# Performance work log

Measured on AMD Instinct MI355X. Metric: run time of the kernel, lower is better.

The kernel has to match this reference:

```python
import jax, jax.numpy as jnp
import numpy as np

NNODES = 512   # sensors/nodes
WIN    = 64    # window_size (input features per node)
NH     = 64    # nhidden
NG     = 3     # ngnn iterations
BATCH  = 1024
OUT    = 32    # out_channels
EPS    = 1e-5  # BatchNorm1d eps


def setup_inputs() -> dict:
    key = jax.random.key(0)
    ks = jax.random.split(key, 8)
    X = jax.random.normal(ks[0], (BATCH, NNODES, WIN), jnp.float32)
    adj_const = jax.random.uniform(ks[1], (NNODES, NNODES), jnp.float32)
    # GCN layer 1 per gnn-iteration: window -> nhidden
    W1 = 0.05 * jax.random.normal(ks[2], (NG, WIN, NH), jnp.float32)
    b1 = jnp.zeros((NG, NH), jnp.float32)
    g1 = jnp.ones((NG, NNODES), jnp.float32)
    be1 = jnp.zeros((NG, NNODES), jnp.float32)
    # GCN layer 2 per gnn-iteration: nhidden -> nhidden
    W2 = 0.05 * jax.random.normal(ks[3], (NG, NH, NH), jnp.float32)
    b2 = jnp.zeros((NG, NH), jnp.float32)
    g2 = jnp.ones((NG, NNODES), jnp.float32)
    be2 = jnp.zeros((NG, NNODES), jnp.float32)
    Wfc = 0.05 * jax.random.normal(ks[4], (NG * NH, OUT), jnp.float32)
    bfc = jnp.zeros((OUT,), jnp.float32)
    return dict(X=X, adj_const=adj_const, W1=W1, b1=b1, g1=g1, be1=be1,
                W2=W2, b2=b2, g2=g2, be2=be2, Wfc=Wfc, bfc=bfc)


def _bn_nodes(h, gamma, beta):
    # torch BatchNorm1d(nnodes) on [B, N, F]: normalize per node channel over (B, F)
    mean = jnp.mean(h, axis=(0, 2), keepdims=True)
    var = jnp.var(h, axis=(0, 2), keepdims=True)
    return (h - mean) * jax.lax.rsqrt(var + EPS) * gamma[None, :, None] + beta[None, :, None]


def reference(X, adj_const, W1, b1, g1, be1, W2, b2, g2, be2, Wfc, bfc):
    # ConstantGraph returns the constant adjacency; z = ones - eye kills self-loops
    adj = adj_const * (1.0 - jnp.eye(NNODES, dtype=X.dtype))
    outs = []
    for i in range(NG):
        # GCNLayer: aggregate over neighbors then linear project
        h = jnp.einsum('nm,bmw->bnw', adj, X) @ W1[i] + b1[i]   # [B,N,NH]
        h = jax.nn.relu(h)
        h = _bn_nodes(h, g1[i], be1[i])
        skip = jnp.min(h, axis=1)                                # [B,NH]
        h = jnp.einsum('nm,bmd->bnd', adj, h) @ W2[i] + b2[i]
        h = jax.nn.relu(h)
        h = _bn_nodes(h, g2[i], be2[i])
        outs.append(jnp.min(h, axis=1) + skip)                   # [B,NH]
    h = jnp.concatenate(outs, axis=1)                            # [B, NG*NH]
    return h @ Wfc + bfc
```

## Files before the change

### kernel.cpp

```cpp
#include <hip/hip_runtime.h>


typedef short  s16x8 __attribute__((ext_vector_type(8)));
typedef float  f32x4 __attribute__((ext_vector_type(4)));

#define NN   512
#define NB   1024
#define NH   64
#define LDT  72

#define MFMA16(a, b, c) __builtin_amdgcn_mfma_f32_16x16x32_bf16((a), (b), (c), 0, 0, 0)

#define GLOAD16(g, l) __builtin_amdgcn_global_load_lds( \
    (const __attribute__((address_space(1))) unsigned*)(g), \
    (__attribute__((address_space(3))) unsigned*)(l), 16, 0, 0)

__device__ __forceinline__ unsigned short f2bf(float f) {
  union { float f; unsigned u; } v; v.f = f;
  unsigned r = v.u + 0x7fffu + ((v.u >> 16) & 1u);
  return (unsigned short)(r >> 16);
}
__device__ __forceinline__ float bf2f(unsigned short h) {
  union { unsigned u; float f; } v; v.u = ((unsigned)h) << 16;
  return v.f;
}

__global__ void k_prep_adj(const float* __restrict__ adj, unsigned short* __restrict__ adjbf) {
  int idx = blockIdx.x * 256 + threadIdx.x;
  int n = idx >> 9, m = idx & 511;
  float v = adj[idx];
  if (n == m) v = 0.f;
  adjbf[idx] = f2bf(v);
}

__global__ void k_prep_w(const float* __restrict__ W1, const float* __restrict__ W2,
                         unsigned short* __restrict__ W1t, unsigned short* __restrict__ W2t) {
  int idx = blockIdx.x * 256 + threadIdx.x;
  int i = idx >> 12, rc_ = idx & 4095;
  int src = (i << 12) + ((rc_ & 63) << 6) + (rc_ >> 6);
  W1t[idx] = f2bf(W1[src]);
  W2t[idx] = f2bf(W2[src]);
}

__global__ __launch_bounds__(256)
void k_transpose_x(const float* __restrict__ X, unsigned short* __restrict__ Xt) {
  __shared__ unsigned short T[64 * LDT];
  int blk = blockIdx.x; int b = blk >> 3; int m0 = (blk & 7) << 6;
  int t = threadIdx.x; int r = t >> 2, seg = t & 3;
  const float* src = X + ((size_t)b * NN + m0 + r) * NH + seg * 16;
#pragma unroll
  for (int e = 0; e < 16; ++e) T[(seg * 16 + e) * LDT + r] = f2bf(src[e]);
  __syncthreads();
  unsigned short* dst = Xt + ((size_t)b * NH + r) * NN + m0 + seg * 16;
  const unsigned short* sT = &T[r * LDT + seg * 16];
  *(s16x8*)dst       = *(const s16x8*)sT;
  *(s16x8*)(dst + 8) = *(const s16x8*)(sT + 8);
}

__global__ __launch_bounds__(512)
void k_gnn1(const unsigned short* __restrict__ Xt, const unsigned short* __restrict__ adjbf,
            const unsigned short* __restrict__ W1t, const float* __restrict__ b1,
            unsigned short* __restrict__ H1T, float* __restrict__ SS1, float* __restrict__ SQ1) {
  __shared__ unsigned short Ab[2][2][4096];
  __shared__ unsigned short Bb[2][8192];
  int h = blockIdx.x;
  int blk = (h & 7) * 256 + (h >> 3);
  int bp = blk >> 2, n0 = (blk & 3) << 7;
  int b0 = bp * 2, b1v = bp * 2 + 1;
  int t = threadIdx.x, lane = t & 63, wid = t >> 6;
  int wf = wid & 1, wn = wid >> 1;
  int arow = wid * 8 + (lane >> 3);
  int swz = ((lane & 7) ^ (arow & 7)) << 3;
  const unsigned short* aS0 = Xt + ((size_t)b0  * NH + arow) * NN + swz;
  const unsigned short* aS1 = Xt + ((size_t)b1v * NH + arow) * NN + swz;
  const unsigned short* bS0 = adjbf + (size_t)(n0 + arow) * NN + swz;
  const unsigned short* bS1 = adjbf + (size_t)(n0 + 64 + arow) * NN + swz;

  GLOAD16(aS0, &Ab[0][0][wid * 512]);
  GLOAD16(aS1, &Ab[1][0][wid * 512]);
  GLOAD16(bS0, &Bb[0][wid * 512]);
  GLOAD16(bS1, &Bb[0][4096 + wid * 512]);
  __syncthreads();

  f32x4 acc[2][2][2] = {};
  for (int kt = 0; kt < 8; ++kt) {
    int cur = kt & 1;
    if (kt < 7) {
      int off = (kt + 1) * 64;
      GLOAD16(aS0 + off, &Ab[0][cur ^ 1][wid * 512]);
      GLOAD16(aS1 + off, &Ab[1][cur ^ 1][wid * 512]);
      GLOAD16(bS0 + off, &Bb[cur ^ 1][wid * 512]);
      GLOAD16(bS1 + off, &Bb[cur ^ 1][4096 + wid * 512]);
    }
    const unsigned short* B = Bb[cur];
#pragma unroll
    for (int kk = 0; kk < 2; ++kk) {
      int ks = (lane >> 4) + kk * 4;
      int ra0 = wf * 32 + (lane & 15), ra1 = ra0 + 16;
      int rb0 = wn * 32 + (lane & 15), rb1 = rb0 + 16;
      s16x8 bf0 = *(const s16x8*)&B[rb0 * 64 + ((ks ^ (rb0 & 7)) << 3)];
      s16x8 bf1 = *(const s16x8*)&B[rb1 * 64 + ((ks ^ (rb1 & 7)) << 3)];
#pragma unroll
      for (int bs = 0; bs < 2; ++bs) {
        const unsigned short* A = Ab[bs][cur];
        s16x8 a0 = *(const s16x8*)&A[ra0 * 64 + ((ks ^ (ra0 & 7)) << 3)];
        s16x8 a1 = *(const s16x8*)&A[ra1 * 64 + ((ks ^ (ra1 & 7)) << 3)];
        acc[bs][0][0] = MFMA16(a0, bf0, acc[bs][0][0]);
        acc[bs][1][0] = MFMA16(a1, bf0, acc[bs][1][0]);
        acc[bs][0][1] = MFMA16(a0, bf1, acc[bs][0][1]);
        acc[bs][1][1] = MFMA16(a1, bf1, acc[bs][1][1]);
      }
    }
    __syncthreads();
  }
#pragma unroll
  for (int bs = 0; bs < 2; ++bs) {
    unsigned short* T = Bb[bs];
#pragma unroll
    for (int fi = 0; fi < 2; ++fi)
#pragma unroll
      for (int fj = 0; fj < 2; ++fj) {
        int nl = wn * 32 + fj * 16 + (lane & 15);
        int w0 = wf * 32 + fi * 16 + (lane >> 4) * 4;
        ushort4 p;
        p.x = f2bf(acc[bs][fi][fj][0]); p.y = f2bf(acc[bs][fi][fj][1]);
        p.z = f2bf(acc[bs][fi][fj][2]); p.w = f2bf(acc[bs][fi][fj][3]);
        *(ushort4*)&T[nl * 64 + (((w0 >> 3) ^ (nl & 7)) << 3) + (w0 & 7)] = p;
      }
  }
#pragma unroll
  for (int j = 0; j < 3; ++j) {
    unsigned short* dstp = (j == 0) ? &Ab[0][0][wid * 512]
                         : (j == 1) ? &Ab[0][1][wid * 512] : &Ab[1][0][wid * 512];
    const unsigned short* gsrc = W1t + j * 4096 + (wid * 8 + (lane >> 3)) * 64
                               + (((lane & 7) ^ (lane >> 3)) << 3);
    GLOAD16(gsrc, dstp);
  }
  __syncthreads();
  int nrow = wid * 16 + (lane & 15);
  s16x8 aT[2][2];
#pragma unroll
  for (int bs = 0; bs < 2; ++bs)
#pragma unroll
    for (int kk = 0; kk < 2; ++kk) {
      int ks = (lane >> 4) + kk * 4;
      aT[bs][kk] = *(const s16x8*)&Bb[bs][nrow * 64 + ((ks ^ (nrow & 7)) << 3)];
    }
#pragma unroll
  for (int i = 0; i < 3; ++i) {
    const unsigned short* w1p = (i == 0) ? Ab[0][0] : (i == 1) ? Ab[0][1] : Ab[1][0];
    s16x8 bw[2][4];
#pragma unroll
    for (int kk = 0; kk < 2; ++kk) {
      int ks = (lane >> 4) + kk * 4;
#pragma unroll
      for (int fd = 0; fd < 4; ++fd) {
        int fr = fd * 16 + (lane & 15);
        bw[kk][fd] = *(const s16x8*)&w1p[fr * 64 + ((ks ^ (fr & 7)) << 3)];
      }
    }
    f32x4 acc2[2][4] = {};
#pragma unroll
    for (int bs = 0; bs < 2; ++bs)
#pragma unroll
      for (int kk = 0; kk < 2; ++kk) {
        acc2[bs][0] = MFMA16(aT[bs][kk], bw[kk][0], acc2[bs][0]);
        acc2[bs][1] = MFMA16(aT[bs][kk], bw[kk][1], acc2[bs][1]);
        acc2[bs][2] = MFMA16(aT[bs][kk], bw[kk][2], acc2[bs][2]);
        acc2[bs][3] = MFMA16(aT[bs][kk], bw[kk][3], acc2[bs][3]);
      }
    unsigned short* H1i = H1T + (size_t)i * 33554432u;
    float svr[4] = {0.f, 0.f, 0.f, 0.f}, sqr[4] = {0.f, 0.f, 0.f, 0.f};
#pragma unroll
    for (int bs = 0; bs < 2; ++bs) {
      int bcur = bs == 0 ? b0 : b1v;
#pragma unroll
      for (int fd = 0; fd < 4; ++fd) {
        int f = fd * 16 + (lane & 15);
        float bia = b1[i * 64 + f];
        float x0 = fmaxf(acc2[bs][fd][0] + bia, 0.f);
        float x1 = fmaxf(acc2[bs][fd][1] + bia, 0.f);
        float x2 = fmaxf(acc2[bs][fd][2] + bia, 0.f);
        float x3 = fmaxf(acc2[bs][fd][3] + bia, 0.f);
        svr[0] += x0; svr[1] += x1; svr[2] += x2; svr[3] += x3;
        sqr[0] += x0 * x0; sqr[1] += x1 * x1; sqr[2] += x2 * x2; sqr[3] += x3 * x3;
        ushort4 p;
        p.x = f2bf(x0); p.y = f2bf(x1); p.z = f2bf(x2); p.w = f2bf(x3);
        *(ushort4*)&H1i[((size_t)bcur * NH + f) * NN + n0 + nrow - (lane & 15) + (lane >> 4) * 4] = p;
      }
    }
#pragma unroll
    for (int rr = 0; rr < 4; ++rr) {
      float sv = svr[rr], qv = sqr[rr];
      sv += __shfl_xor(sv, 1); sv += __shfl_xor(sv, 2); sv += __shfl_xor(sv, 4); sv += __shfl_xor(sv, 8);
      qv += __shfl_xor(qv, 1); qv += __shfl_xor(qv, 2); qv += __shfl_xor(qv, 4); qv += __shfl_xor(qv, 8);
      if ((lane & 15) == 0) {
        int n = n0 + wid * 16 + (lane >> 4) * 4 + rr;
        atomicAdd(&SS1[i * 512 + n], sv);
        atomicAdd(&SQ1[i * 512 + n], qv);
      }
    }
  }
}

__global__ __launch_bounds__(256)
void k_adjb(const unsigned short* __restrict__ adjbf,
            const float* __restrict__ Ssum, const float* __restrict__ Ssq,
            const float* __restrict__ g, const float* __restrict__ be,
            unsigned short* __restrict__ adjB, float* __restrict__ rc,
            float* __restrict__ A1, float* __restrict__ C1) {
  __shared__ float red[256];
  int n = blockIdx.x, t = threadIdx.x;
  float acc = 0.f;
#pragma unroll
  for (int hh = 0; hh < 2; ++hh) {
    int m = t + hh * 256;
    float mean = Ssum[m] * (1.f / 65536.f);
    float var  = Ssq[m] * (1.f / 65536.f) - mean * mean;
    float a = g[m] * rsqrtf(var + 1e-5f);
    float c = be[m] - mean * a;
    if (n == 0) { A1[m] = a; C1[m] = c; }
    float av = bf2f(adjbf[n * NN + m]);
    adjB[n * NN + m] = f2bf(av * a);
    acc += av * c;
  }
  red[t] = acc; __syncthreads();
  for (int s = 128; s > 0; s >>= 1) { if (t < s) red[t] += red[t + s]; __syncthreads(); }
  if (t == 0) rc[n] = red[0];
}

__global__ __launch_bounds__(256)
void k_minrow_out(const unsigned short* __restrict__ Ht,
                  const float* __restrict__ Ssum, const float* __restrict__ Ssq,
                  const float* __restrict__ g, const float* __restrict__ be,
                  const float* __restrict__ skip_i, float* __restrict__ outs, int i) {
  int t = threadIdx.x, lane = t & 63, wid = t >> 6;
  int row = blockIdx.x * 4 + wid;
  int b = row >> 6, d = row & 63;
  s16x8 hv = *(const s16x8*)(Ht + (size_t)row * NN + lane * 8);
  float m = 1e30f;
#pragma unroll
  for (int e = 0; e < 8; ++e) {
    int mm = lane * 8 + e;
    float mean = Ssum[mm] * (1.f / 65536.f);
    float var  = Ssq[mm] * (1.f / 65536.f) - mean * mean;
    float a = g[mm] * rsqrtf(var + 1e-5f);
    float c = be[mm] - mean * a;
    m = fminf(m, a * bf2f((unsigned short)hv[e]) + c);
  }
#pragma unroll
  for (int off = 1; off < 64; off <<= 1) m = fminf(m, __shfl_xor(m, off));
  if (lane == 0) outs[(size_t)b * 192 + i * 64 + d] = m + skip_i[row];
}

__global__ __launch_bounds__(512)
void k_layer2(const unsigned short* __restrict__ H1t_i, const unsigned short* __restrict__ adjB,
              const float* __restrict__ rc, const unsigned short* __restrict__ W2t_i,
              const float* __restrict__ b2_i, unsigned short* __restrict__ H2t,
              float* __restrict__ Ssum2, float* __restrict__ Ssq2,
              const float* __restrict__ A1v, const float* __restrict__ C1v,
              float* __restrict__ skip_i) {
  __shared__ unsigned short Ab[2][2][4096];
  __shared__ unsigned short Bb[2][8192];
  __shared__ float acs[512], ccs[512];
  int h = blockIdx.x;
  int blk = (h & 7) * 256 + (h >> 3);
  int bp = blk >> 2, n0 = (blk & 3) << 7;
  int b0 = bp * 2, b1v = bp * 2 + 1;
  int t = threadIdx.x, lane = t & 63, wid = t >> 6;
  int wf = wid & 1, wn = wid >> 1;
  bool do_min = (n0 == 0);
  int arow = wid * 8 + (lane >> 3);
  int swz = ((lane & 7) ^ (arow & 7)) << 3;
  const unsigned short* aS0 = H1t_i + ((size_t)b0  * NH + arow) * NN + swz;
  const unsigned short* aS1 = H1t_i + ((size_t)b1v * NH + arow) * NN + swz;
  const unsigned short* bS0 = adjB + (size_t)(n0 + arow) * NN + swz;
  const unsigned short* bS1 = adjB + (size_t)(n0 + 64 + arow) * NN + swz;
  acs[t] = A1v[t]; ccs[t] = C1v[t];
  float rcv[2];
  rcv[0] = rc[n0 + wn * 32 + (lane & 15)];
  rcv[1] = rc[n0 + wn * 32 + 16 + (lane & 15)];

  GLOAD16(aS0, &Ab[0][0][wid * 512]);
  GLOAD16(aS1, &Ab[1][0][wid * 512]);
  GLOAD16(bS0, &Bb[0][wid * 512]);
  GLOAD16(bS1, &Bb[0][4096 + wid * 512]);
  __syncthreads();

  float mn0 = 1e30f, mn1 = 1e30f;
  f32x4 acc[2][2][2] = {};
  for (int kt = 0; kt < 8; ++kt) {
    int cur = kt & 1;
    if (kt < 7) {
      int off = (kt + 1) * 64;
      GLOAD16(aS0 + off, &Ab[0][cur ^ 1][wid * 512]);
      GLOAD16(aS1 + off, &Ab[1][cur ^ 1][wid * 512]);
      GLOAD16(bS0 + off, &Bb[cur ^ 1][wid * 512]);
      GLOAD16(bS1 + off, &Bb[cur ^ 1][4096 + wid * 512]);
    }
    if (do_min) {
      int s2 = ((lane & 7) ^ (arow & 7)) << 3;
      s16x8 av0 = *(const s16x8*)&Ab[0][cur][arow * 64 + s2];
      s16x8 av1 = *(const s16x8*)&Ab[1][cur][arow * 64 + s2];
      int m0 = kt * 64 + ((lane & 7) << 3);
#pragma unroll
      for (int e = 0; e < 8; ++e) {
        mn0 = fminf(mn0, acs[m0 + e] * bf2f((unsigned short)av0[e]) + ccs[m0 + e]);
        mn1 = fminf(mn1, acs[m0 + e] * bf2f((unsigned short)av1[e]) + ccs[m0 + e]);
      }
    }
    const unsigned short* B = Bb[cur];
#pragma unroll
    for (int kk = 0; kk < 2; ++kk) {
      int ks = (lane >> 4) + kk * 4;
      int ra0 = wf * 32 + (lane & 15), ra1 = ra0 + 16;
      int rb0 = wn * 32 + (lane & 15), rb1 = rb0 + 16;
      s16x8 bf0 = *(const s16x8*)&B[rb0 * 64 + ((ks ^ (rb0 & 7)) << 3)];
      s16x8 bf1 = *(const s16x8*)&B[rb1 * 64 + ((ks ^ (rb1 & 7)) << 3)];
#pragma unroll
      for (int bs = 0; bs < 2; ++bs) {
        const unsigned short* A = Ab[bs][cur];
        s16x8 a0 = *(const s16x8*)&A[ra0 * 64 + ((ks ^ (ra0 & 7)) << 3)];
        s16x8 a1 = *(const s16x8*)&A[ra1 * 64 + ((ks ^ (ra1 & 7)) << 3)];
        acc[bs][0][0] = MFMA16(a0, bf0, acc[bs][0][0]);
        acc[bs][1][0] = MFMA16(a1, bf0, acc[bs][1][0]);
        acc[bs][0][1] = MFMA16(a0, bf1, acc[bs][0][1]);
        acc[bs][1][1] = MFMA16(a1, bf1, acc[bs][1][1]);
      }
    }
    __syncthreads();
  }
  if (do_min) {
    mn0 = fminf(mn0, __shfl_xor(mn0, 1)); mn1 = fminf(mn1, __shfl_xor(mn1, 1));
    mn0 = fminf(mn0, __shfl_xor(mn0, 2)); mn1 = fminf(mn1, __shfl_xor(mn1, 2));
    mn0 = fminf(mn0, __shfl_xor(mn0, 4)); mn1 = fminf(mn1, __shfl_xor(mn1, 4));
    if ((lane & 7) == 0) {
      skip_i[b0 * 64 + arow] = mn0;
      skip_i[b1v * 64 + arow] = mn1;
    }
  }
#pragma unroll
  for (int bs = 0; bs < 2; ++bs) {
    unsigned short* Gt = Bb[bs];
#pragma unroll
    for (int fi = 0; fi < 2; ++fi)
#pragma unroll
      for (int fj = 0; fj < 2; ++fj) {
        int n  = wn * 32 + fj * 16 + (lane & 15);
        int f0 = wf * 32 + fi * 16 + (lane >> 4) * 4;
        ushort4 p;
        p.x = f2bf(acc[bs][fi][fj][0] + rcv[fj]); p.y = f2bf(acc[bs][fi][fj][1] + rcv[fj]);
        p.z = f2bf(acc[bs][fi][fj][2] + rcv[fj]); p.w = f2bf(acc[bs][fi][fj][3] + rcv[fj]);
        *(ushort4*)&Gt[n * 64 + (((f0 >> 3) ^ (n & 7)) << 3) + (f0 & 7)] = p;
      }
  }
  __syncthreads();
  s16x8 w2f[2][4];
  float bb[4];
#pragma unroll
  for (int kk = 0; kk < 2; ++kk)
#pragma unroll
    for (int fd = 0; fd < 4; ++fd)
      w2f[kk][fd] = *(const s16x8*)&W2t_i[(fd * 16 + (lane & 15)) * 64 + kk * 32 + (lane >> 4) * 8];
#pragma unroll
  for (int fd = 0; fd < 4; ++fd) bb[fd] = b2_i[fd * 16 + (lane & 15)];

  int nrow = wid * 16 + (lane & 15);
  f32x4 acc2[2][4] = {};
#pragma unroll
  for (int bs = 0; bs < 2; ++bs)
#pragma unroll
    for (int kk = 0; kk < 2; ++kk) {
      int ks = (lane >> 4) + kk * 4;
      s16x8 a = *(const s16x8*)&Bb[bs][nrow * 64 + ((ks ^ (nrow & 7)) << 3)];
      acc2[bs][0] = MFMA16(a, w2f[kk][0], acc2[bs][0]);
      acc2[bs][1] = MFMA16(a, w2f[kk][1], acc2[bs][1]);
      acc2[bs][2] = MFMA16(a, w2f[kk][2], acc2[bs][2]);
      acc2[bs][3] = MFMA16(a, w2f[kk][3], acc2[bs][3]);
    }
  float svr[4] = {0.f, 0.f, 0.f, 0.f}, sqr[4] = {0.f, 0.f, 0.f, 0.f};
#pragma unroll
  for (int bs = 0; bs < 2; ++bs) {
    int bcur = bs == 0 ? b0 : b1v;
#pragma unroll
    for (int fd = 0; fd < 4; ++fd) {
      int d  = fd * 16 + (lane & 15);
      int nw = n0 + wid * 16 + (lane >> 4) * 4;
      float x0 = fmaxf(acc2[bs][fd][0] + bb[fd], 0.f);
      float x1 = fmaxf(acc2[bs][fd][1] + bb[fd], 0.f);
      float x2 = fmaxf(acc2[bs][fd][2] + bb[fd], 0.f);
      float x3 = fmaxf(acc2[bs][fd][3] + bb[fd], 0.f);
      svr[0] += x0; svr[1] += x1; svr[2] += x2; svr[3] += x3;
      sqr[0] += x0 * x0; sqr[1] += x1 * x1; sqr[2] += x2 * x2; sqr[3] += x3 * x3;
      ushort4 p;
      p.x = f2bf(x0); p.y = f2bf(x1); p.z = f2bf(x2); p.w = f2bf(x3);
      *(ushort4*)&H2t[((size_t)bcur * NH + d) * NN + nw] = p;
    }
  }
#pragma unroll
  for (int rr = 0; rr < 4; ++rr) {
    float sv = svr[rr], qv = sqr[rr];
    sv += __shfl_xor(sv, 1); sv += __shfl_xor(sv, 2); sv += __shfl_xor(sv, 4); sv += __shfl_xor(sv, 8);
    qv += __shfl_xor(qv, 1); qv += __shfl_xor(qv, 2); qv += __shfl_xor(qv, 4); qv += __shfl_xor(qv, 8);
    if ((lane & 15) == 0) {
      int n = n0 + wid * 16 + (lane >> 4) * 4 + rr;
      atomicAdd(&Ssum2[n], sv);
      atomicAdd(&Ssq2[n], qv);
    }
  }
}

__global__ __launch_bounds__(256)
void k_fc(const float* __restrict__ outs, const float* __restrict__ Wfc,
          const float* __restrict__ bfc, float* __restrict__ out) {
  int t = threadIdx.x;
  int b = blockIdx.x * 8 + (t >> 5), o = t & 31;
  float acc = bfc[o];
  const float* orow = outs + (size_t)b * 192;
  for (int j = 0; j < 192; ++j) acc += orow[j] * Wfc[j * 32 + o];
  out[b * 32 + o] = acc;
}

extern "C" void kernel_launch(void* const* d_in, const int* in_sizes, int n_in,
                              void* d_out, int out_size, void* d_ws, size_t ws_size,
                              hipStream_t stream) {
  const float* X   = (const float*)d_in[0];
  const float* adj = (const float*)d_in[1];
  const float* W1  = (const float*)d_in[2];
  const float* b1  = (const float*)d_in[3];
  const float* g1  = (const float*)d_in[4];
  const float* be1 = (const float*)d_in[5];
  const float* W2  = (const float*)d_in[6];
  const float* b2  = (const float*)d_in[7];
  const float* g2  = (const float*)d_in[8];
  const float* be2 = (const float*)d_in[9];
  const float* Wfc = (const float*)d_in[10];
  const float* bfc = (const float*)d_in[11];
  float* out = (float*)d_out;

  char* ws = (char*)d_ws;
  size_t off = 0;
  auto alloc = [&](size_t bytes) {
    char* p = ws + off; off += (bytes + 255) & ~(size_t)255; return p;
  };
  unsigned short* ADJBF = (unsigned short*)alloc(512 * 512 * 2);
  unsigned short* ADJB  = (unsigned short*)alloc(512 * 512 * 2);
  unsigned short* W1T   = (unsigned short*)alloc(3 * 4096 * 2);
  unsigned short* W2T   = (unsigned short*)alloc(3 * 4096 * 2);
  float* SS1 = (float*)alloc(3 * 512 * 4);
  float* SQ1 = (float*)alloc(3 * 512 * 4);
  float* SS2 = (float*)alloc(3 * 512 * 4);
  float* SQ2 = (float*)alloc(3 * 512 * 4);
  float* A1  = (float*)alloc(3 * 512 * 4);
  float* C1  = (float*)alloc(3 * 512 * 4);
  float* RC  = (float*)alloc(512 * 4);
  float* SKIP = (float*)alloc(3 * 1024 * 64 * 4);
  float* OUTS = (float*)alloc(1024 * 192 * 4);
  unsigned short* XT  = (unsigned short*)alloc((size_t)1024 * 64 * 512 * 2);
  unsigned short* H1T = (unsigned short*)alloc((size_t)3 * 1024 * 64 * 512 * 2);
  unsigned short* H2T = XT;

  hipMemsetAsync(SS1, 0, 4 * 3 * 512 * 4, stream);

  k_prep_adj<<<1024, 256, 0, stream>>>(adj, ADJBF);
  k_prep_w<<<48, 256, 0, stream>>>(W1, W2, W1T, W2T);
  k_transpose_x<<<8192, 256, 0, stream>>>(X, XT);
  k_gnn1<<<2048, 512, 0, stream>>>(XT, ADJBF, W1T, b1, H1T, SS1, SQ1);

  for (int i = 0; i < 3; ++i) {
    k_adjb<<<512, 256, 0, stream>>>(ADJBF, SS1 + i * 512, SQ1 + i * 512,
                                    g1 + i * 512, be1 + i * 512, ADJB, RC,
                                    A1 + i * 512, C1 + i * 512);
    k_layer2<<<2048, 512, 0, stream>>>(H1T + (size_t)i * 33554432u, ADJB, RC,
                                       W2T + i * 4096, b2 + i * 64, H2T,
                                       SS2 + i * 512, SQ2 + i * 512,
                                       A1 + i * 512, C1 + i * 512, SKIP + i * 65536);
    k_minrow_out<<<16384, 256, 0, stream>>>(H2T, SS2 + i * 512, SQ2 + i * 512,
                                            g2 + i * 512, be2 + i * 512,
                                            SKIP + i * 65536, OUTS, i);
  }
  k_fc<<<128, 256, 0, stream>>>(OUTS, Wfc, bfc, out);
}
```

Measured before the change: 531.2 us.

## Recompute layer-1 hidden in layer2 from shared aggregate instead of storing H1

```diff
diff --git a/kernel.cpp b/kernel.cpp
--- a/kernel.cpp
+++ b/kernel.cpp
@@ -60,7 +60,7 @@
 __global__ __launch_bounds__(512)
 void k_gnn1(const unsigned short* __restrict__ Xt, const unsigned short* __restrict__ adjbf,
             const unsigned short* __restrict__ W1t, const float* __restrict__ b1,
-            unsigned short* __restrict__ H1T, float* __restrict__ SS1, float* __restrict__ SQ1) {
+            unsigned short* __restrict__ Tg, float* __restrict__ SS1, float* __restrict__ SQ1) {
   __shared__ unsigned short Ab[2][2][4096];
   __shared__ unsigned short Bb[2][8192];
   int h = blockIdx.x;
@@ -115,6 +115,21 @@
   }
 #pragma unroll
   for (int bs = 0; bs < 2; ++bs) {
+    int bcur = bs == 0 ? b0 : b1v;
+#pragma unroll
+    for (int fi = 0; fi < 2; ++fi)
+#pragma unroll
+      for (int fj = 0; fj < 2; ++fj) {
+        int n = n0 + wn * 32 + fj * 16 + (lane & 15);
+        int w = wf * 32 + fi * 16 + (lane >> 4) * 4;
+        ushort4 pk;
+        pk.x = f2bf(acc[bs][fi][fj][0]); pk.y = f2bf(acc[bs][fi][fj][1]);
+        pk.z = f2bf(acc[bs][fi][fj][2]); pk.w = f2bf(acc[bs][fi][fj][3]);
+        *(ushort4*)&Tg[((size_t)bcur * NN + n) * NH + w] = pk;
+      }
+  }
+#pragma unroll
+  for (int bs = 0; bs < 2; ++bs) {
     unsigned short* T = Bb[bs];
 #pragma unroll
     for (int fi = 0; fi < 2; ++fi)
@@ -169,26 +184,18 @@
         acc2[bs][2] = MFMA16(aT[bs][kk], bw[kk][2], acc2[bs][2]);
         acc2[bs][3] = MFMA16(aT[bs][kk], bw[kk][3], acc2[bs][3]);
       }
-    unsigned short* H1i = H1T + (size_t)i * 33554432u;
     float svr[4] = {0.f, 0.f, 0.f, 0.f}, sqr[4] = {0.f, 0.f, 0.f, 0.f};
 #pragma unroll
-    for (int bs = 0; bs < 2; ++bs) {
-      int bcur = bs == 0 ? b0 : b1v;
+    for (int bs = 0; bs < 2; ++bs)
 #pragma unroll
       for (int fd = 0; fd < 4; ++fd) {
-        int f = fd * 16 + (lane & 15);
-        float bia = b1[i * 64 + f];
-        float x0 = fmaxf(acc2[bs][fd][0] + bia, 0.f);
-        float x1 = fmaxf(acc2[bs][fd][1] + bia, 0.f);
-        float x2 = fmaxf(acc2[bs][fd][2] + bia, 0.f);
-        float x3 = fmaxf(acc2[bs][fd][3] + bia, 0.f);
-        svr[0] += x0; svr[1] += x1; svr[2] += x2; svr[3] += x3;
-        sqr[0] += x0 * x0; sqr[1] += x1 * x1; sqr[2] += x2 * x2; sqr[3] += x3 * x3;
-        ushort4 p;
-        p.x = f2bf(x0); p.y = f2bf(x1); p.z = f2bf(x2); p.w = f2bf(x3);
-        *(ushort4*)&H1i[((size_t)bcur * NH + f) * NN + n0 + nrow - (lane & 15) + (lane >> 4) * 4] = p;
-      }
-    }
+        float bia = b1[i * 64 + fd * 16 + (lane & 15)];
+#pragma unroll
+        for (int rr = 0; rr < 4; ++rr) {
+          float x = fmaxf(acc2[bs][fd][rr] + bia, 0.f);
+          svr[rr] += x; sqr[rr] += x * x;
+        }
+      }
 #pragma unroll
     for (int rr = 0; rr < 4; ++rr) {
       float sv = svr[rr], qv = sqr[rr];
@@ -253,107 +260,136 @@
   if (lane == 0) outs[(size_t)b * 192 + i * 64 + d] = m + skip_i[row];
 }
 
-__global__ __launch_bounds__(512)
-void k_layer2(const unsigned short* __restrict__ H1t_i, const unsigned short* __restrict__ adjB,
-              const float* __restrict__ rc, const unsigned short* __restrict__ W2t_i,
-              const float* __restrict__ b2_i, unsigned short* __restrict__ H2t,
+__global__ __launch_bounds__(256)
+void k_layer2(const unsigned short* __restrict__ Tg, const unsigned short* __restrict__ adjB,
+              const float* __restrict__ rc,
+              const unsigned short* __restrict__ W1t_i, const float* __restrict__ b1_i,
+              const unsigned short* __restrict__ W2t_i, const float* __restrict__ b2_i,
+              unsigned short* __restrict__ H2t,
               float* __restrict__ Ssum2, float* __restrict__ Ssq2,
               const float* __restrict__ A1v, const float* __restrict__ C1v,
               float* __restrict__ skip_i) {
-  __shared__ unsigned short Ab[2][2][4096];
+  __shared__ unsigned short Tch[2][4096];
   __shared__ unsigned short Bb[2][8192];
+  __shared__ unsigned short H1c[4096];
   __shared__ float acs[512], ccs[512];
   int h = blockIdx.x;
-  int blk = (h & 7) * 256 + (h >> 3);
-  int bp = blk >> 2, n0 = (blk & 3) << 7;
-  int b0 = bp * 2, b1v = bp * 2 + 1;
+  int blk = (h & 7) * 512 + (h >> 3);
+  int b = blk >> 2, n0 = (blk & 3) << 7;
   int t = threadIdx.x, lane = t & 63, wid = t >> 6;
   int wf = wid & 1, wn = wid >> 1;
   bool do_min = (n0 == 0);
-  int arow = wid * 8 + (lane >> 3);
-  int swz = ((lane & 7) ^ (arow & 7)) << 3;
-  const unsigned short* aS0 = H1t_i + ((size_t)b0  * NH + arow) * NN + swz;
-  const unsigned short* aS1 = H1t_i + ((size_t)b1v * NH + arow) * NN + swz;
-  const unsigned short* bS0 = adjB + (size_t)(n0 + arow) * NN + swz;
-  const unsigned short* bS1 = adjB + (size_t)(n0 + 64 + arow) * NN + swz;
-  acs[t] = A1v[t]; ccs[t] = C1v[t];
-  float rcv[2];
-  rcv[0] = rc[n0 + wn * 32 + (lane & 15)];
-  rcv[1] = rc[n0 + wn * 32 + 16 + (lane & 15)];
-
-  GLOAD16(aS0, &Ab[0][0][wid * 512]);
-  GLOAD16(aS1, &Ab[1][0][wid * 512]);
-  GLOAD16(bS0, &Bb[0][wid * 512]);
-  GLOAD16(bS1, &Bb[0][4096 + wid * 512]);
+  acs[t] = A1v[t]; acs[t + 256] = A1v[t + 256];
+  ccs[t] = C1v[t]; ccs[t + 256] = C1v[t + 256];
+  s16x8 w1f[2];
+  float b1r[4];
+#pragma unroll
+  for (int kk = 0; kk < 2; ++kk)
+    w1f[kk] = *(const s16x8*)&W1t_i[(wid * 16 + (lane & 15)) * 64 + kk * 32 + (lane >> 4) * 8];
+#pragma unroll
+  for (int rr = 0; rr < 4; ++rr) b1r[rr] = b1_i[wid * 16 + (lane >> 4) * 4 + rr];
+  int lrow = lane >> 3, lsl = lane & 7;
+  const unsigned short* tBase = Tg + (size_t)b * (NN * NH);
+#pragma unroll
+  for (int q = 0; q < 2; ++q) {
+    int r = wid * 16 + q * 8 + lrow;
+    GLOAD16(tBase + (size_t)r * NH + ((lsl ^ (r & 7)) << 3), &Tch[0][r * 64]);
+  }
+#pragma unroll
+  for (int q = 0; q < 4; ++q) {
+    int r = wid * 32 + q * 8 + lrow;
+    GLOAD16(adjB + (size_t)(n0 + r) * NN + ((lsl ^ (r & 7)) << 3), &Bb[0][r * 64]);
+  }
   __syncthreads();
 
-  float mn0 = 1e30f, mn1 = 1e30f;
-  f32x4 acc[2][2][2] = {};
+  float mn[4] = {1e30f, 1e30f, 1e30f, 1e30f};
+  f32x4 acc[2][4] = {};
   for (int kt = 0; kt < 8; ++kt) {
     int cur = kt & 1;
     if (kt < 7) {
-      int off = (kt + 1) * 64;
-      GLOAD16(aS0 + off, &Ab[0][cur ^ 1][wid * 512]);
-      GLOAD16(aS1 + off, &Ab[1][cur ^ 1][wid * 512]);
-      GLOAD16(bS0 + off, &Bb[cur ^ 1][wid * 512]);
-      GLOAD16(bS1 + off, &Bb[cur ^ 1][4096 + wid * 512]);
-    }
-    if (do_min) {
-      int s2 = ((lane & 7) ^ (arow & 7)) << 3;
-      s16x8 av0 = *(const s16x8*)&Ab[0][cur][arow * 64 + s2];
-      s16x8 av1 = *(const s16x8*)&Ab[1][cur][arow * 64 + s2];
-      int m0 = kt * 64 + ((lane & 7) << 3);
-#pragma unroll
-      for (int e = 0; e < 8; ++e) {
-        mn0 = fminf(mn0, acs[m0 + e] * bf2f((unsigned short)av0[e]) + ccs[m0 + e]);
-        mn1 = fminf(mn1, acs[m0 + e] * bf2f((unsigned short)av1[e]) + ccs[m0 + e]);
-      }
-    }
-    const unsigned short* B = Bb[cur];
-#pragma unroll
-    for (int kk = 0; kk < 2; ++kk) {
-      int ks = (lane >> 4) + kk * 4;
-      int ra0 = wf * 32 + (lane & 15), ra1 = ra0 + 16;
-      int rb0 = wn * 32 + (lane & 15), rb1 = rb0 + 16;
-      s16x8 bf0 = *(const s16x8*)&B[rb0 * 64 + ((ks ^ (rb0 & 7)) << 3)];
-      s16x8 bf1 = *(const s16x8*)&B[rb1 * 64 + ((ks ^ (rb1 & 7)) << 3)];
-#pragma unroll
-      for (int bs = 0; bs < 2; ++bs) {
-        const unsigned short* A = Ab[bs][cur];
-        s16x8 a0 = *(const s16x8*)&A[ra0 * 64 + ((ks ^ (ra0 & 7)) << 3)];
-        s16x8 a1 = *(const s16x8*)&A[ra1 * 64 + ((ks ^ (ra1 & 7)) << 3)];
-        acc[bs][0][0] = MFMA16(a0, bf0, acc[bs][0][0]);
-        acc[bs][1][0] = MFMA16(a1, bf0, acc[bs][1][0]);
-        acc[bs][0][1] = MFMA16(a0, bf1, acc[bs][0][1]);
-        acc[bs][1][1] = MFMA16(a1, bf1, acc[bs][1][1]);
+      int koff = (kt + 1) * 64;
+#pragma unroll
+      for (int q = 0; q < 2; ++q) {
+        int r = wid * 16 + q * 8 + lrow;
+        GLOAD16(tBase + (size_t)(koff + r) * NH + ((lsl ^ (r & 7)) << 3), &Tch[cur ^ 1][r * 64]);
+      }
+#pragma unroll
+      for (int q = 0; q < 4; ++q) {
+        int r = wid * 32 + q * 8 + lrow;
+        GLOAD16(adjB + (size_t)(n0 + r) * NN + koff + ((lsl ^ (r & 7)) << 3), &Bb[cur ^ 1][r * 64]);
+      }
+    }
+    {
+      const unsigned short* Tc = Tch[cur];
+#pragma unroll
+      for (int mt = 0; mt < 4; ++mt) {
+        f32x4 rg = {};
+#pragma unroll
+        for (int kk = 0; kk < 2; ++kk) {
+          int ks = (lane >> 4) + kk * 4;
+          int mr = mt * 16 + (lane & 15);
+          s16x8 tf = *(const s16x8*)&Tc[mr * 64 + ((ks ^ (mr & 7)) << 3)];
+          rg = MFMA16(w1f[kk], tf, rg);
+        }
+        int mloc = mt * 16 + (lane & 15);
+        int mglob = kt * 64 + mloc;
+        float ac = acs[mglob], cc = ccs[mglob];
+#pragma unroll
+        for (int rr = 0; rr < 4; ++rr) {
+          float x = fmaxf(rg[rr] + b1r[rr], 0.f);
+          if (do_min) mn[rr] = fminf(mn[rr], ac * x + cc);
+          int f = wid * 16 + (lane >> 4) * 4 + rr;
+          H1c[f * 64 + (((mloc >> 3) ^ (f & 7)) << 3) + (mloc & 7)] = f2bf(x);
+        }
       }
     }
     __syncthreads();
+    {
+      const unsigned short* B = Bb[cur];
+#pragma unroll
+      for (int kk = 0; kk < 2; ++kk) {
+        int ks = (lane >> 4) + kk * 4;
+        int ra0 = wf * 32 + (lane & 15), ra1 = ra0 + 16;
+        s16x8 a0 = *(const s16x8*)&H1c[ra0 * 64 + ((ks ^ (ra0 & 7)) << 3)];
+        s16x8 a1 = *(const s16x8*)&H1c[ra1 * 64 + ((ks ^ (ra1 & 7)) << 3)];
+#pragma unroll
+        for (int j = 0; j < 4; ++j) {
+          int rb = wn * 64 + j * 16 + (lane & 15);
+          s16x8 bf = *(const s16x8*)&B[rb * 64 + ((ks ^ (rb & 7)) << 3)];
+          acc[0][j] = MFMA16(a0, bf, acc[0][j]);
+          acc[1][j] = MFMA16(a1, bf, acc[1][j]);
+        }
+      }
+    }
+    __syncthreads();
   }
   if (do_min) {
-    mn0 = fminf(mn0, __shfl_xor(mn0, 1)); mn1 = fminf(mn1, __shfl_xor(mn1, 1));
-    mn0 = fminf(mn0, __shfl_xor(mn0, 2)); mn1 = fminf(mn1, __shfl_xor(mn1, 2));
-    mn0 = fminf(mn0, __shfl_xor(mn0, 4)); mn1 = fminf(mn1, __shfl_xor(mn1, 4));
-    if ((lane & 7) == 0) {
-      skip_i[b0 * 64 + arow] = mn0;
-      skip_i[b1v * 64 + arow] = mn1;
-    }
-  }
-#pragma unroll
-  for (int bs = 0; bs < 2; ++bs) {
-    unsigned short* Gt = Bb[bs];
-#pragma unroll
-    for (int fi = 0; fi < 2; ++fi)
-#pragma unroll
-      for (int fj = 0; fj < 2; ++fj) {
-        int n  = wn * 32 + fj * 16 + (lane & 15);
-        int f0 = wf * 32 + fi * 16 + (lane >> 4) * 4;
-        ushort4 p;
-        p.x = f2bf(acc[bs][fi][fj][0] + rcv[fj]); p.y = f2bf(acc[bs][fi][fj][1] + rcv[fj]);
-        p.z = f2bf(acc[bs][fi][fj][2] + rcv[fj]); p.w = f2bf(acc[bs][fi][fj][3] + rcv[fj]);
-        *(ushort4*)&Gt[n * 64 + (((f0 >> 3) ^ (n & 7)) << 3) + (f0 & 7)] = p;
-      }
-  }
+#pragma unroll
+    for (int rr = 0; rr < 4; ++rr) {
+      mn[rr] = fminf(mn[rr], __shfl_xor(mn[rr], 1));
+      mn[rr] = fminf(mn[rr], __shfl_xor(mn[rr], 2));
+      mn[rr] = fminf(mn[rr], __shfl_xor(mn[rr], 4));
+      mn[rr] = fminf(mn[rr], __shfl_xor(mn[rr], 8));
+    }
+    if ((lane & 15) == 0) {
+#pragma unroll
+      for (int rr = 0; rr < 4; ++rr)
+        skip_i[b * 64 + wid * 16 + (lane >> 4) * 4 + rr] = mn[rr];
+    }
+  }
+  unsigned short* Gt = Bb[0];
+#pragma unroll
+  for (int fi = 0; fi < 2; ++fi)
+#pragma unroll
+    for (int j = 0; j < 4; ++j) {
+      int n  = wn * 64 + j * 16 + (lane & 15);
+      int f0 = wf * 32 + fi * 16 + (lane >> 4) * 4;
+      float rv = rc[n0 + n];
+      ushort4 p;
+      p.x = f2bf(acc[fi][j][0] + rv); p.y = f2bf(acc[fi][j][1] + rv);
+      p.z = f2bf(acc[fi][j][2] + rv); p.w = f2bf(acc[fi][j][3] + rv);
+      *(ushort4*)&Gt[n * 64 + (((f0 >> 3) ^ (n & 7)) << 3) + (f0 & 7)] = p;
+    }
   __syncthreads();
   s16x8 w2f[2][4];
   float bb[4];
@@ -365,47 +401,43 @@
 #pragma unroll
   for (int fd = 0; fd < 4; ++fd) bb[fd] = b2_i[fd * 16 + (lane & 15)];
 
-  int nrow = wid * 16 + (lane & 15);
-  f32x4 acc2[2][4] = {};
-#pragma unroll
-  for (int bs = 0; bs < 2; ++bs)
+#pragma unroll
+  for (int ns = 0; ns < 2; ++ns) {
+    int nrow = wid * 32 + ns * 16 + (lane & 15);
+    f32x4 acc2[4] = {};
 #pragma unroll
     for (int kk = 0; kk < 2; ++kk) {
-      int ks = (lane >> 4) + kk * 4;
-      s16x8 a = *(const s16x8*)&Bb[bs][nrow * 64 + ((ks ^ (nrow & 7)) << 3)];
-      acc2[bs][0] = MFMA16(a, w2f[kk][0], acc2[bs][0]);
-      acc2[bs][1] = MFMA16(a, w2f[kk][1], acc2[bs][1]);
-      acc2[bs][2] = MFMA16(a, w2f[kk][2], acc2[bs][2]);
-      acc2[bs][3] = MFMA16(a, w2f[kk][3], acc2[bs][3]);
-    }
-  float svr[4] = {0.f, 0.f, 0.f, 0.f}, sqr[4] = {0.f, 0.f, 0.f, 0.f};
-#pragma unroll
-  for (int bs = 0; bs < 2; ++bs) {
-    int bcur = bs == 0 ? b0 : b1v;
+      int es = (lane >> 4) + kk * 4;
+      s16x8 a = *(const s16x8*)&Gt[nrow * 64 + ((es ^ (nrow & 7)) << 3)];
+      acc2[0] = MFMA16(a, w2f[kk][0], acc2[0]);
+      acc2[1] = MFMA16(a, w2f[kk][1], acc2[1]);
+      acc2[2] = MFMA16(a, w2f[kk][2], acc2[2]);
+      acc2[3] = MFMA16(a, w2f[kk][3], acc2[3]);
+    }
+    float svr[4] = {0.f, 0.f, 0.f, 0.f}, sqr[4] = {0.f, 0.f, 0.f, 0.f};
+    int nw = n0 + wid * 32 + ns * 16 + (lane >> 4) * 4;
 #pragma unroll
     for (int fd = 0; fd < 4; ++fd) {
-      int d  = fd * 16 + (lane & 15);
-      int nw = n0 + wid * 16 + (lane >> 4) * 4;
-      float x0 = fmaxf(acc2[bs][fd][0] + bb[fd], 0.f);
-      float x1 = fmaxf(acc2[bs][fd][1] + bb[fd], 0.f);
-      float x2 = fmaxf(acc2[bs][fd][2] + bb[fd], 0.f);
-      float x3 = fmaxf(acc2[bs][fd][3] + bb[fd], 0.f);
+      int d = fd * 16 + (lane & 15);
+      float x0 = fmaxf(acc2[fd][0] + bb[fd], 0.f);
+      float x1 = fmaxf(acc2[fd][1] + bb[fd], 0.f);
+      float x2 = fmaxf(acc2[fd][2] + bb[fd], 0.f);
+      float x3 = fmaxf(acc2[fd][3] + bb[fd], 0.f);
       svr[0] += x0; svr[1] += x1; svr[2] += x2; svr[3] += x3;
       sqr[0] += x0 * x0; sqr[1] += x1 * x1; sqr[2] += x2 * x2; sqr[3] += x3 * x3;
       ushort4 p;
       p.x = f2bf(x0); p.y = f2bf(x1); p.z = f2bf(x2); p.w = f2bf(x3);
-      *(ushort4*)&H2t[((size_t)bcur * NH + d) * NN + nw] = p;
-    }
-  }
-#pragma unroll
-  for (int rr = 0; rr < 4; ++rr) {
-    float sv = svr[rr], qv = sqr[rr];
-    sv += __shfl_xor(sv, 1); sv += __shfl_xor(sv, 2); sv += __shfl_xor(sv, 4); sv += __shfl_xor(sv, 8);
-    qv += __shfl_xor(qv, 1); qv += __shfl_xor(qv, 2); qv += __shfl_xor(qv, 4); qv += __shfl_xor(qv, 8);
-    if ((lane & 15) == 0) {
-      int n = n0 + wid * 16 + (lane >> 4) * 4 + rr;
-      atomicAdd(&Ssum2[n], sv);
-      atomicAdd(&Ssq2[n], qv);
+      *(ushort4*)&H2t[((size_t)b * NH + d) * NN + nw] = p;
+    }
+#pragma unroll
+    for (int rr = 0; rr < 4; ++rr) {
+      float sv = svr[rr], qv = sqr[rr];
+      sv += __shfl_xor(sv, 1); sv += __shfl_xor(sv, 2); sv += __shfl_xor(sv, 4); sv += __shfl_xor(sv, 8);
+      qv += __shfl_xor(qv, 1); qv += __shfl_xor(qv, 2); qv += __shfl_xor(qv, 4); qv += __shfl_xor(qv, 8);
+      if ((lane & 15) == 0) {
+        atomicAdd(&Ssum2[nw + rr], sv);
+        atomicAdd(&Ssq2[nw + rr], qv);
+      }
     }
   }
 }
@@ -457,7 +489,7 @@
   float* SKIP = (float*)alloc(3 * 1024 * 64 * 4);
   float* OUTS = (float*)alloc(1024 * 192 * 4);
   unsigned short* XT  = (unsigned short*)alloc((size_t)1024 * 64 * 512 * 2);
-  unsigned short* H1T = (unsigned short*)alloc((size_t)3 * 1024 * 64 * 512 * 2);
+  unsigned short* TG  = (unsigned short*)alloc((size_t)1024 * 512 * 64 * 2);
   unsigned short* H2T = XT;
 
   hipMemsetAsync(SS1, 0, 4 * 3 * 512 * 4, stream);
@@ -465,13 +497,13 @@
   k_prep_adj<<<1024, 256, 0, stream>>>(adj, ADJBF);
   k_prep_w<<<48, 256, 0, stream>>>(W1, W2, W1T, W2T);
   k_transpose_x<<<8192, 256, 0, stream>>>(X, XT);
-  k_gnn1<<<2048, 512, 0, stream>>>(XT, ADJBF, W1T, b1, H1T, SS1, SQ1);
+  k_gnn1<<<2048, 512, 0, stream>>>(XT, ADJBF, W1T, b1, TG, SS1, SQ1);
 
   for (int i = 0; i < 3; ++i) {
     k_adjb<<<512, 256, 0, stream>>>(ADJBF, SS1 + i * 512, SQ1 + i * 512,
                                     g1 + i * 512, be1 + i * 512, ADJB, RC,
                                     A1 + i * 512, C1 + i * 512);
-    k_layer2<<<2048, 512, 0, stream>>>(H1T + (size_t)i * 33554432u, ADJB, RC,
+    k_layer2<<<4096, 256, 0, stream>>>(TG, ADJB, RC, W1T + i * 4096, b1 + i * 64,
                                        W2T + i * 4096, b2 + i * 64, H2T,
                                        SS2 + i * 512, SQ2 + i * 512,
                                        A1 + i * 512, C1 + i * 512, SKIP + i * 65536);
```

Measured after the change: 661.2 us. 1.24x slower.
